# Performance work log

Hardware: AMD Instinct MI355X
Metric: run time of the kernel (lower is better)

Reference implementation:

```python
import jax, jax.numpy as jnp
import numpy as np
import math

B, T, E, H = 64, 256, 1024, 16
HD = E // H  # 64
EPS = 1e-5


def layernorm(x, g, b):
    mu = jnp.mean(x, axis=-1, keepdims=True)
    var = jnp.mean(jnp.square(x - mu), axis=-1, keepdims=True)
    return (x - mu) * jax.lax.rsqrt(var + EPS) * g + b


def setup_inputs() -> dict:
    key = jax.random.key(0)
    ks = jax.random.split(key, 10)
    s = 0.02
    return {
        "x": jax.random.normal(ks[0], (B, T, E), dtype=jnp.float32),
        "ln1_g": jnp.ones((E,), jnp.float32),
        "ln1_b": jnp.zeros((E,), jnp.float32),
        "wk": jax.random.normal(ks[1], (H, E, HD), jnp.float32) * s,
        "wq": jax.random.normal(ks[2], (H, E, HD), jnp.float32) * s,
        "wv": jax.random.normal(ks[3], (H, E, HD), jnp.float32) * s,
        "w_proj": jax.random.normal(ks[4], (E, E), jnp.float32) * s,
        "b_proj": jnp.zeros((E,), jnp.float32),
        "ln2_g": jnp.ones((E,), jnp.float32),
        "ln2_b": jnp.zeros((E,), jnp.float32),
        "w1": jax.random.normal(ks[5], (E, E), jnp.float32) * s,
        "b1": jnp.zeros((E,), jnp.float32),
        "w2": jax.random.normal(ks[6], (E, E), jnp.float32) * s,
        "b2": jnp.zeros((E,), jnp.float32),
    }


def reference(x, ln1_g, ln1_b, wk, wq, wv, w_proj, b_proj, ln2_g, ln2_b, w1, b1, w2, b2):
    # --- multi-head causal attention on LN1(x) ---
    h = layernorm(x, ln1_g, ln1_b)
    k = jnp.einsum('bte,hed->bhtd', h, wk)
    q = jnp.einsum('bte,hed->bhtd', h, wq)
    v = jnp.einsum('bte,hed->bhtd', h, wv)
    # NOTE: original computes k @ q^T (K.Q^T), not the standard Q.K^T -- kept faithful
    scores = jnp.einsum('bhtd,bhsd->bhts', k, q) / math.sqrt(HD)
    mask = jnp.tril(jnp.ones((T, T), dtype=bool))
    scores = jnp.where(mask, scores, -jnp.inf)
    attn_w = jax.nn.softmax(scores, axis=-1)  # dropout = identity in eval
    attn = jnp.einsum('bhts,bhsd->bhtd', attn_w, v)
    attn = attn.transpose(0, 2, 1, 3).reshape(B, T, E)  # concat heads
    x = x + attn @ w_proj + b_proj
    # --- feed-forward on LN2(x) ---
    h2 = layernorm(x, ln2_g, ln2_b)
    ff = jax.nn.relu(h2 @ w1 + b1) @ w2 + b2
    return x + ff
```

## Files before the change

### kernel.cpp

```cpp
#include <hip/hip_runtime.h>

typedef unsigned int u32;
typedef unsigned short u16;
typedef __attribute__((ext_vector_type(8))) short bf16x8;
typedef __attribute__((ext_vector_type(4))) float f32x4;

#define GLOBAL_AS __attribute__((address_space(1)))
#define LDS_AS    __attribute__((address_space(3)))

#define B_   64
#define T_   256
#define E_   1024
#define H_   16
#define HD_  64
#define NTOK (B_*T_)
#define K_   1024
#define LNEPS 1e-5f

__device__ __forceinline__ u16 f2bf(float f){
  u32 x = __float_as_uint(f);
  u32 r = x + 0x7fffu + ((x >> 16) & 1u);
  return (u16)(r >> 16);
}
__device__ __forceinline__ u16 f2bf_trunc(float f){
  return (u16)(__float_as_uint(f) >> 16);
}
__device__ __forceinline__ u32 pack2(float a, float b){
  return (u32)f2bf(a) | ((u32)f2bf(b) << 16);
}

__device__ __forceinline__ void gload16(const u16* g, u16* l){
  __builtin_amdgcn_global_load_lds((const GLOBAL_AS void*)g, (LDS_AS void*)l, 16, 0, 0);
}

__global__ __launch_bounds__(256) void ln_bf16_kernel(
    const float* __restrict__ x, const float* __restrict__ g,
    const float* __restrict__ b, u16* __restrict__ o)
{
  int lane  = threadIdx.x & 63;
  int token = (blockIdx.x << 2) + (threadIdx.x >> 6);
  const float4* xr = (const float4*)(x + (size_t)token * E_);
  float4 v[4];
  float s = 0.f, ss = 0.f;
  #pragma unroll
  for (int i = 0; i < 4; ++i){
    v[i] = xr[lane + 64 * i];
    s += v[i].x + v[i].y + v[i].z + v[i].w;
    ss = fmaf(v[i].x, v[i].x, fmaf(v[i].y, v[i].y,
         fmaf(v[i].z, v[i].z, fmaf(v[i].w, v[i].w, ss))));
  }
  #pragma unroll
  for (int off = 32; off > 0; off >>= 1){
    s  += __shfl_xor(s,  off);
    ss += __shfl_xor(ss, off);
  }
  float mu   = s * (1.f / E_);
  float var  = ss * (1.f / E_) - mu * mu;
  float rstd = rsqrtf(var + LNEPS);
  const float4* gr = (const float4*)g;
  const float4* br = (const float4*)b;
  uint2* orow = (uint2*)(o + (size_t)token * E_);
  #pragma unroll
  for (int i = 0; i < 4; ++i){
    float4 gg = gr[lane + 64 * i], bb = br[lane + 64 * i];
    float y0 = (v[i].x - mu) * rstd * gg.x + bb.x;
    float y1 = (v[i].y - mu) * rstd * gg.y + bb.y;
    float y2 = (v[i].z - mu) * rstd * gg.z + bb.z;
    float y3 = (v[i].w - mu) * rstd * gg.w + bb.w;
    orow[lane + 64 * i] = make_uint2(pack2(y0, y1), pack2(y2, y3));
  }
}

__global__ __launch_bounds__(256) void convq_kernel(
    const float* __restrict__ wk, const float* __restrict__ wq,
    const float* __restrict__ wv, u16* __restrict__ o)
{
  __shared__ float tile[64 * 68];
  const int zh = blockIdx.x, z = zh >> 4, h = zh & 15;
  const int k0 = blockIdx.y << 6;
  const float* w = (z == 0 ? wk : z == 1 ? wq : wv) + (size_t)h * (E_ * HD_);
  const int t = threadIdx.x;
  {
    int kr = t >> 2, d0 = (t & 3) << 4;
    const float4* src = (const float4*)(w + (size_t)(k0 + kr) * HD_ + d0);
    #pragma unroll
    for (int i = 0; i < 4; ++i)
      *(float4*)(tile + kr * 68 + d0 + 4 * i) = src[i];
  }
  __syncthreads();
  {
    const size_t nb32 = (size_t)zh * 32 + (k0 >> 5);
    #pragma unroll
    for (int u = 0; u < 2; ++u) {
      int cid = t * 2 + u;
      int dd = cid >> 3, kc = cid & 7;
      u32 wd[4];
      #pragma unroll
      for (int e2 = 0; e2 < 4; ++e2)
        wd[e2] = pack2(tile[(kc * 8 + 2 * e2) * 68 + dd],
                       tile[(kc * 8 + 2 * e2 + 1) * 68 + dd]);
      u16* dst = o + (nb32 + (kc >> 2)) * 2048 + (size_t)(dd >> 4) * 512
                   + (size_t)(((kc & 3) << 4) + (dd & 15)) * 8;
      *(uint4*)dst = make_uint4(wd[0], wd[1], wd[2], wd[3]);
    }
  }
}

__global__ __launch_bounds__(256) void convt_kernel(
    const float* __restrict__ w, u16* __restrict__ o)
{
  __shared__ float tile[64 * 68];
  const int n0 = blockIdx.x << 6, k0 = blockIdx.y << 6;
  const int t = threadIdx.x;
  {
    int kr = t >> 2, nn = (t & 3) << 4;
    const float4* src = (const float4*)(w + (size_t)(k0 + kr) * E_ + n0 + nn);
    #pragma unroll
    for (int i = 0; i < 4; ++i)
      *(float4*)(tile + kr * 68 + nn + 4 * i) = src[i];
  }
  __syncthreads();
  {
    const size_t nb32 = (size_t)(n0 >> 6) * 32 + (k0 >> 5);
    #pragma unroll
    for (int u = 0; u < 2; ++u) {
      int cid = t * 2 + u;
      int dd = cid >> 3, kc = cid & 7;
      u32 wd[4];
      #pragma unroll
      for (int e2 = 0; e2 < 4; ++e2)
        wd[e2] = pack2(tile[(kc * 8 + 2 * e2) * 68 + dd],
                       tile[(kc * 8 + 2 * e2 + 1) * 68 + dd]);
      u16* dst = o + (nb32 + (kc >> 2)) * 2048 + (size_t)(dd >> 4) * 512
                   + (size_t)(((kc & 3) << 4) + (dd & 15)) * 8;
      *(uint4*)dst = make_uint4(wd[0], wd[1], wd[2], wd[3]);
    }
  }
}

#define MF4(I, AV, BV)                                                               \
  acc[I][0] = __builtin_amdgcn_mfma_f32_16x16x32_bf16(AV, BV[0], acc[I][0], 0, 0, 0);\
  acc[I][1] = __builtin_amdgcn_mfma_f32_16x16x32_bf16(AV, BV[1], acc[I][1], 0, 0, 0);\
  acc[I][2] = __builtin_amdgcn_mfma_f32_16x16x32_bf16(AV, BV[2], acc[I][2], 0, 0, 0);\
  acc[I][3] = __builtin_amdgcn_mfma_f32_16x16x32_bf16(AV, BV[3], acc[I][3], 0, 0, 0);

#define BLOADS(BV, SS) {                                                      \
    const u16* bp_ = Bp + (size_t)(SS) * 2048;                                \
    BV[0] = *(const bf16x8*)(bp_);                                            \
    BV[1] = *(const bf16x8*)(bp_ + 512);                                      \
    BV[2] = *(const bf16x8*)(bp_ + 1024);                                     \
    BV[3] = *(const bf16x8*)(bp_ + 1536);                                     \
  }

#define MSLICE(SLOT, DST, KA, DO_STAGE, BV, BL, VM) {                         \
    const u16* As_ = lds + (SLOT) * 8192;                                     \
    bf16x8 a0 = *(const bf16x8*)(As_ + aoffb);                                \
    bf16x8 a1 = *(const bf16x8*)(As_ + aoffb + 512);                          \
    bf16x8 a2 = *(const bf16x8*)(As_ + aoffb + 1024);                         \
    bf16x8 a3 = *(const bf16x8*)(As_ + aoffb + 1536);                         \
    if (DO_STAGE) {                                                           \
      u16* d_ = lds + (DST) * 8192;                                           \
      gload16(Ag0 + (KA), d_ + tid * 8);                                      \
      gload16(Ag1 + (KA), d_ + 4096 + tid * 8);                               \
    }                                                                         \
    __builtin_amdgcn_s_barrier();                                             \
    asm volatile("s_waitcnt lgkmcnt(0)" ::: "memory");                        \
    __builtin_amdgcn_sched_barrier(0);                                        \
    __builtin_amdgcn_s_setprio(1);                                            \
    MF4(0, a0, BV) MF4(1, a1, BV) MF4(2, a2, BV) MF4(3, a3, BV)               \
    __builtin_amdgcn_s_setprio(0);                                            \
    a0 = *(const bf16x8*)(As_ + aoffb + 2048);                                \
    a1 = *(const bf16x8*)(As_ + aoffb + 2560);                                \
    a2 = *(const bf16x8*)(As_ + aoffb + 3072);                                \
    a3 = *(const bf16x8*)(As_ + aoffb + 3584);                                \
    asm volatile("s_waitcnt lgkmcnt(0)" ::: "memory");                        \
    __builtin_amdgcn_sched_barrier(0);                                        \
    __builtin_amdgcn_s_setprio(1);                                            \
    MF4(4, a0, BV) MF4(5, a1, BV) MF4(6, a2, BV) MF4(7, a3, BV)               \
    __builtin_amdgcn_s_setprio(0);                                            \
    BL;                                                                       \
    VM;                                                                       \
    __builtin_amdgcn_s_barrier();                                             \
    asm volatile("" ::: "memory");                                            \
  }

#define VM12 asm volatile("s_waitcnt vmcnt(12)" ::: "memory")
#define VM10 asm volatile("s_waitcnt vmcnt(10)" ::: "memory")
#define VM8  asm volatile("s_waitcnt vmcnt(8)"  ::: "memory")

template<int MODE>
__global__ __launch_bounds__(512, 2) void mgemm_kernel(
    const u16* __restrict__ A, const u16* __restrict__ Bt,
    const float* __restrict__ bias, const float* __restrict__ resid,
    float* __restrict__ Cf, u16* __restrict__ Cb, u16* __restrict__ Cb2)
{
  __shared__ __align__(16) u16 lds[65536];

  const int tid = threadIdx.x, lane = tid & 63, wid = tid >> 6;
  const int wm = wid >> 2, wn = wid & 3;
  const int l15 = lane & 15, quad = lane >> 4;

  const int b = (int)blockIdx.x;
  const int xcd = b & 7, ib = b >> 3;
  const int row0 = ((xcd << 3) + (ib & 7)) << 8;
  const int col0 = (ib >> 3) << 8;

  const int sc   = (tid & 7) ^ ((tid >> 3) & 7);
  const int srow = 2 * (tid >> 3) + (sc >> 2);
  const int skof = (sc & 3) << 3;
  const u16* Ag0 = A + (size_t)(row0 + srow) * K_ + skof;
  const u16* Ag1 = Ag0 + (size_t)128 * K_;

  const int rhalf = l15 >> 1;
  const int cph   = ((((l15 & 1) << 2) | quad) ^ rhalf);
  const int aoffb = wm * 4096 + rhalf * 64 + cph * 8;

  const u16* Bp = Bt + (size_t)((col0 >> 6) + wn) * 65536 + lane * 8;

  f32x4 acc[8][4];
  #pragma unroll
  for (int i = 0; i < 8; ++i)
    #pragma unroll
    for (int j = 0; j < 4; ++j)
      acc[i][j] = (f32x4){0.f, 0.f, 0.f, 0.f};

  bf16x8 bE[4], bO[4];

  #pragma unroll
  for (int t3 = 0; t3 < 3; ++t3) {
    u16* d_ = lds + t3 * 8192;
    gload16(Ag0 + t3 * 32, d_ + tid * 8);
    gload16(Ag1 + t3 * 32, d_ + 4096 + tid * 8);
  }
  BLOADS(bE, 0)
  BLOADS(bO, 1)
  asm volatile("s_waitcnt vmcnt(12)" ::: "memory");
  __builtin_amdgcn_s_barrier();
  asm volatile("" ::: "memory");

  #pragma unroll 1
  for (int s = 0; s < 28; s += 2) {
    MSLICE(s & 3, (s + 3) & 3, (s + 3) * 32, 1, bE, BLOADS(bE, s + 2), VM12)
    MSLICE((s + 1) & 3, (s + 4) & 3, (s + 4) * 32, 1, bO, BLOADS(bO, s + 3), VM12)
  }
  MSLICE(0, 3, 31 * 32, 1, bE, BLOADS(bE, 30), VM12)
  MSLICE(1, 0, 0,       0, bO, BLOADS(bO, 31), VM10)
  MSLICE(2, 0, 0,       0, bE, (void)0,        VM8 )
  MSLICE(3, 0, 0,       0, bO, (void)0,        (void)0)

  if (MODE == 1 || MODE == 3) {
    const int rbase = row0 + wm * 128;
    #pragma unroll
    for (int j = 0; j < 4; ++j) {
      const int n = col0 + wn * 64 + j * 16 + l15;
      const float bn = bias[n];
      #pragma unroll
      for (int i = 0; i < 8; ++i)
        #pragma unroll
        for (int r = 0; r < 4; ++r) {
          const int row = rbase + i * 16 + quad * 4 + r;
          const size_t idx = (size_t)row * E_ + n;
          float v = acc[i][j][r] + bn;
          if (MODE == 1) Cf[idx] = v + resid[idx];
          else           Cf[idx] = v + Cf[idx];
        }
    }
    return;
  }

  u16* ep = lds + wid * 8192;
  const int nb0 = col0 + wn * 64;

  if (MODE == 2) {
    #pragma unroll
    for (int j = 0; j < 4; ++j) {
      const float bn = bias[nb0 + j * 16 + l15];
      #pragma unroll
      for (int i = 0; i < 8; ++i)
        #pragma unroll
        for (int r = 0; r < 4; ++r)
          ep[(i*16 + quad*4 + r) * 64 + j*16 + l15] =
              f2bf(fmaxf(acc[i][j][r] + bn, 0.f));
    }
    __syncthreads();
    const int rbase = row0 + wm * 128;
    #pragma unroll
    for (int it = 0; it < 16; ++it) {
      const int tl = it * 8 + (lane >> 3), c = lane & 7;
      uint4 v = *(const uint4*)(ep + tl * 64 + c * 8);
      *(uint4*)(Cb + (size_t)(rbase + tl) * E_ + nb0 + c * 8) = v;
    }
    return;
  }

  const int z = nb0 >> 10, hh = (nb0 >> 6) & 15;
  const int rows0 = row0 + wm * 128;
  const int bb = rows0 >> 8, tb0 = rows0 & 255;
  if (z < 2) {
    #pragma unroll
    for (int i = 0; i < 8; ++i)
      #pragma unroll
      for (int j = 0; j < 4; ++j)
        #pragma unroll
        for (int r = 0; r < 4; ++r)
          ep[(i*16 + quad*4 + r) * 64 + j*16 + l15] = f2bf(acc[i][j][r]);
    __syncthreads();
    u16* out = (z == 0 ? Cb : Cb2) + ((size_t)(bb * H_ + hh) * T_ + tb0) * HD_;
    #pragma unroll
    for (int it = 0; it < 16; ++it) {
      const int tl = it * 8 + (lane >> 3), c = lane & 7;
      uint4 v = *(const uint4*)(ep + tl * 64 + c * 8);
      *(uint4*)(out + (size_t)tl * HD_ + c * 8) = v;
    }
  } else {
    #pragma unroll
    for (int i = 0; i < 8; ++i)
      #pragma unroll
      for (int j = 0; j < 4; ++j)
        #pragma unroll
        for (int r = 0; r < 4; ++r) {
          const int tl = i*16 + quad*4 + r, d = j*16 + l15;
          const int phys = (tl >> 3) ^ (d & 15);
          ep[d * 128 + phys * 8 + (tl & 7)] = f2bf(acc[i][j][r]);
        }
    __syncthreads();
    u16* out = (u16*)Cf + ((size_t)(bb * H_ + hh) * HD_) * T_;
    #pragma unroll
    for (int it = 0; it < 16; ++it) {
      const int d = it * 4 + (lane >> 4), c = lane & 15;
      const int phys = c ^ (d & 15);
      uint4 v = *(const uint4*)(ep + d * 128 + phys * 8);
      *(uint4*)(out + (size_t)d * T_ + tb0 + c * 8) = v;
    }
  }
}

__global__ __launch_bounds__(256) void fattn_kernel(
    const u16* __restrict__ kk_, const u16* __restrict__ qq_,
    const u16* __restrict__ vt_, u16* __restrict__ out)
{
  __shared__ __align__(16) u16 Pb[4][64 * 72];
  const int tid = threadIdx.x, lane = tid & 63, wv = tid >> 6;
  const int bh = blockIdx.x * 4 + wv;
  const int tblk = blockIdx.y;
  const int l15 = lane & 15, quad = lane >> 4;
  const u16* kb  = kk_ + (size_t)bh * (T_ * HD_);
  const u16* qb  = qq_ + (size_t)bh * (T_ * HD_);
  const u16* vtb = vt_ + (size_t)bh * (HD_ * T_);
  u16* Pw = Pb[wv];

  bf16x8 kf[4][2];
  #pragma unroll
  for (int i = 0; i < 4; ++i)
    #pragma unroll
    for (int c = 0; c < 2; ++c)
      kf[i][c] = *(const bf16x8*)(kb + (size_t)(tblk*64 + i*16 + l15) * HD_ + c*32 + quad*8);

  f32x4 o[4][4];
  float mrow[4][4], lrow[4][4];
  #pragma unroll
  for (int i = 0; i < 4; ++i) {
    #pragma unroll
    for (int j = 0; j < 4; ++j) o[i][j] = (f32x4){0.f, 0.f, 0.f, 0.f};
    #pragma unroll
    for (int r = 0; r < 4; ++r) { mrow[i][r] = -1e30f; lrow[i][r] = 0.f; }
  }

  for (int sb = 0; sb <= tblk; ++sb) {
    f32x4 S[4][4];
    #pragma unroll
    for (int j = 0; j < 4; ++j) {
      bf16x8 qf0 = *(const bf16x8*)(qb + (size_t)(sb*64 + j*16 + l15) * HD_ +      quad*8);
      bf16x8 qf1 = *(const bf16x8*)(qb + (size_t)(sb*64 + j*16 + l15) * HD_ + 32 + quad*8);
      #pragma unroll
      for (int i = 0; i < 4; ++i) {
        f32x4 t0 = __builtin_amdgcn_mfma_f32_16x16x32_bf16(kf[i][0], qf0,
                       (f32x4){0.f,0.f,0.f,0.f}, 0, 0, 0);
        S[i][j] = __builtin_amdgcn_mfma_f32_16x16x32_bf16(kf[i][1], qf1, t0, 0, 0, 0);
      }
    }
    #pragma unroll
    for (int i = 0; i < 4; ++i)
      #pragma unroll
      for (int j = 0; j < 4; ++j)
        #pragma unroll
        for (int r = 0; r < 4; ++r) {
          float val = S[i][j][r] * 0.125f;
          if (sb == tblk) {
            int tl = i*16 + quad*4 + r, sl = j*16 + l15;
            if (sl > tl) val = -1e30f;
          }
          S[i][j][r] = val;
        }
    #pragma unroll
    for (int i = 0; i < 4; ++i)
      #pragma unroll
      for (int r = 0; r < 4; ++r) {
        float mx = fmaxf(fmaxf(S[i][0][r], S[i][1][r]), fmaxf(S[i][2][r], S[i][3][r]));
        #pragma unroll
        for (int msk = 1; msk < 16; msk <<= 1) mx = fmaxf(mx, __shfl_xor(mx, msk));
        float mn = fmaxf(mrow[i][r], mx);
        float al = __expf(mrow[i][r] - mn);
        mrow[i][r] = mn;
        float sm = 0.f;
        #pragma unroll
        for (int j = 0; j < 4; ++j) {
          float p = __expf(S[i][j][r] - mn);
          S[i][j][r] = p;
          sm += p;
        }
        #pragma unroll
        for (int msk = 1; msk < 16; msk <<= 1) sm += __shfl_xor(sm, msk);
        lrow[i][r] = lrow[i][r] * al + sm;
        #pragma unroll
        for (int jd = 0; jd < 4; ++jd) o[i][jd][r] *= al;
      }
    #pragma unroll
    for (int i = 0; i < 4; ++i)
      #pragma unroll
      for (int j = 0; j < 4; ++j)
        #pragma unroll
        for (int r = 0; r < 4; ++r)
          Pw[(i*16 + quad*4 + r) * 72 + j*16 + l15] = f2bf_trunc(S[i][j][r]);
    __syncthreads();
    bf16x8 pf[4][2];
    #pragma unroll
    for (int i = 0; i < 4; ++i)
      #pragma unroll
      for (int c = 0; c < 2; ++c)
        pf[i][c] = *(const bf16x8*)(Pw + (i*16 + l15) * 72 + c*32 + quad*8);
    #pragma unroll
    for (int jd = 0; jd < 4; ++jd) {
      bf16x8 vf0 = *(const bf16x8*)(vtb + (size_t)(jd*16 + l15) * T_ + sb*64 +      quad*8);
      bf16x8 vf1 = *(const bf16x8*)(vtb + (size_t)(jd*16 + l15) * T_ + sb*64 + 32 + quad*8);
      #pragma unroll
      for (int i = 0; i < 4; ++i) {
        f32x4 t0 = __builtin_amdgcn_mfma_f32_16x16x32_bf16(pf[i][0], vf0, o[i][jd], 0, 0, 0);
        o[i][jd] = __builtin_amdgcn_mfma_f32_16x16x32_bf16(pf[i][1], vf1, t0, 0, 0, 0);
      }
    }
    __syncthreads();
  }

  #pragma unroll
  for (int i = 0; i < 4; ++i)
    #pragma unroll
    for (int r = 0; r < 4; ++r) {
      float inv = 1.0f / lrow[i][r];
      #pragma unroll
      for (int jd = 0; jd < 4; ++jd)
        Pw[(i*16 + quad*4 + r) * 72 + jd*16 + l15] = f2bf(o[i][jd][r] * inv);
    }
  __syncthreads();
  {
    const int b = bh >> 4, h = bh & 15;
    const uint4* pr = (const uint4*)(Pw + lane * 72);
    uint4* og = (uint4*)(out + ((size_t)(b * T_ + tblk*64 + lane)) * E_ + h * HD_);
    #pragma unroll
    for (int k = 0; k < 8; ++k) og[k] = pr[k];
  }
}

extern "C" void kernel_launch(void* const* d_in, const int* in_sizes, int n_in,
                              void* d_out, int out_size, void* d_ws, size_t ws_size,
                              hipStream_t stream) {
  const float* x     = (const float*)d_in[0];
  const float* ln1g  = (const float*)d_in[1];
  const float* ln1b  = (const float*)d_in[2];
  const float* wk    = (const float*)d_in[3];
  const float* wq    = (const float*)d_in[4];
  const float* wv    = (const float*)d_in[5];
  const float* wproj = (const float*)d_in[6];
  const float* bproj = (const float*)d_in[7];
  const float* ln2g  = (const float*)d_in[8];
  const float* ln2b  = (const float*)d_in[9];
  const float* w1    = (const float*)d_in[10];
  const float* b1    = (const float*)d_in[11];
  const float* w2    = (const float*)d_in[12];
  const float* b2    = (const float*)d_in[13];
  float* outp = (float*)d_out;

  char* ws = (char*)d_ws;
  const size_t MB = 1024 * 1024;
  u16* wqkvT  = (u16*)(ws);
  u16* wprojT = (u16*)(ws + 6 * MB);
  u16* w1T    = (u16*)(ws + 8 * MB);
  u16* w2T    = (u16*)(ws + 10 * MB);
  u16* hb     = (u16*)(ws + 16 * MB);
  u16* kbuf   = (u16*)(ws + 48 * MB);
  u16* qbuf   = (u16*)(ws + 80 * MB);
  u16* vtbuf  = (u16*)d_out;

  convq_kernel<<<dim3(48, 16), 256, 0, stream>>>(wk, wq, wv, wqkvT);
  convt_kernel<<<dim3(16, 16), 256, 0, stream>>>(wproj, wprojT);
  convt_kernel<<<dim3(16, 16), 256, 0, stream>>>(w1, w1T);
  convt_kernel<<<dim3(16, 16), 256, 0, stream>>>(w2, w2T);

  ln_bf16_kernel<<<NTOK/4, 256, 0, stream>>>(x, ln1g, ln1b, hb);
  mgemm_kernel<0><<<768, 512, 0, stream>>>(
      hb, wqkvT, nullptr, nullptr, (float*)vtbuf, kbuf, qbuf);
  fattn_kernel<<<dim3(B_*H_/4, 4), 256, 0, stream>>>(kbuf, qbuf, vtbuf, hb);
  mgemm_kernel<1><<<256, 512, 0, stream>>>(
      hb, wprojT, bproj, x, outp, nullptr, nullptr);
  ln_bf16_kernel<<<NTOK/4, 256, 0, stream>>>(outp, ln2g, ln2b, kbuf);
  mgemm_kernel<2><<<256, 512, 0, stream>>>(
      kbuf, w1T, b1, nullptr, nullptr, qbuf, nullptr);
  mgemm_kernel<3><<<256, 512, 0, stream>>>(
      qbuf, w2T, b2, nullptr, outp, nullptr, nullptr);
}
```

Measured before the change: 527.0 us.

## Prefetch next-slice A fragments across barrier in GEMM, drop attention syncthreads

Reworks the GEMM main loop so A fragments for the next k-slice are read from LDS during the current slice's MFMAs, with register double-buffering. This removes the barrier and lgkmcnt wait that sat before each slice's first MFMAs, and the vmcnt thresholds are retuned to match. The attention kernel also drops several __syncthreads around its per-wave P staging buffer, assuming each wave only touches its own Pw region. The cost is extra registers and a risk of LDS read/write races if the slot timing or the per-wave ownership assumptions are wrong.

```diff
diff --git a/kernel.cpp b/kernel.cpp
--- a/kernel.cpp
+++ b/kernel.cpp
@@ -152,41 +152,42 @@
     BV[3] = *(const bf16x8*)(bp_ + 1536);                                     \
   }
 
-#define MSLICE(SLOT, DST, KA, DO_STAGE, BV, BL, VM) {                         \
+#define MSLICE2(SLOT, NSLOT, KA, DO_STAGE, DO_NXT, DO_BL, BS, ACUR, ATMP, ANXT, BV, BNV, VM) { \
     const u16* As_ = lds + (SLOT) * 8192;                                     \
-    bf16x8 a0 = *(const bf16x8*)(As_ + aoffb);                                \
-    bf16x8 a1 = *(const bf16x8*)(As_ + aoffb + 512);                          \
-    bf16x8 a2 = *(const bf16x8*)(As_ + aoffb + 1024);                         \
-    bf16x8 a3 = *(const bf16x8*)(As_ + aoffb + 1536);                         \
+          \
+    ATMP[0] = *(const bf16x8*)(As_ + aoffb + 2048);                           \
+    ATMP[1] = *(const bf16x8*)(As_ + aoffb + 2560);                           \
+    ATMP[2] = *(const bf16x8*)(As_ + aoffb + 3072);                           \
+    ATMP[3] = *(const bf16x8*)(As_ + aoffb + 3584);                           \
     if (DO_STAGE) {                                                           \
-      u16* d_ = lds + (DST) * 8192;                                           \
+      u16* d_ = lds + (((SLOT) + 3) & 3) * 8192;                              \
       gload16(Ag0 + (KA), d_ + tid * 8);                                      \
       gload16(Ag1 + (KA), d_ + 4096 + tid * 8);                               \
     }                                                                         \
-    __builtin_amdgcn_s_barrier();                                             \
-    asm volatile("s_waitcnt lgkmcnt(0)" ::: "memory");                        \
-    __builtin_amdgcn_sched_barrier(0);                                        \
     __builtin_amdgcn_s_setprio(1);                                            \
-    MF4(0, a0, BV) MF4(1, a1, BV) MF4(2, a2, BV) MF4(3, a3, BV)               \
+    MF4(0, ACUR[0], BV) MF4(1, ACUR[1], BV) MF4(2, ACUR[2], BV) MF4(3, ACUR[3], BV) \
     __builtin_amdgcn_s_setprio(0);                                            \
-    a0 = *(const bf16x8*)(As_ + aoffb + 2048);                                \
-    a1 = *(const bf16x8*)(As_ + aoffb + 2560);                                \
-    a2 = *(const bf16x8*)(As_ + aoffb + 3072);                                \
-    a3 = *(const bf16x8*)(As_ + aoffb + 3584);                                \
-    asm volatile("s_waitcnt lgkmcnt(0)" ::: "memory");                        \
-    __builtin_amdgcn_sched_barrier(0);                                        \
+             \
+    if (DO_NXT) {                                                             \
+      const u16* An_ = lds + (NSLOT) * 8192;                                  \
+      ANXT[0] = *(const bf16x8*)(An_ + aoffb);                                \
+      ANXT[1] = *(const bf16x8*)(An_ + aoffb + 512);                          \
+      ANXT[2] = *(const bf16x8*)(An_ + aoffb + 1024);                         \
+      ANXT[3] = *(const bf16x8*)(An_ + aoffb + 1536);                         \
+    }                                                                         \
     __builtin_amdgcn_s_setprio(1);                                            \
-    MF4(4, a0, BV) MF4(5, a1, BV) MF4(6, a2, BV) MF4(7, a3, BV)               \
+    MF4(4, ATMP[0], BV) MF4(5, ATMP[1], BV) MF4(6, ATMP[2], BV) MF4(7, ATMP[3], BV) \
     __builtin_amdgcn_s_setprio(0);                                            \
-    BL;                                                                       \
+    if (DO_BL) { BLOADS(BNV, BS) }                                            \
     VM;                                                                       \
     __builtin_amdgcn_s_barrier();                                             \
+    __builtin_amdgcn_sched_barrier(0);                                        \
     asm volatile("" ::: "memory");                                            \
   }
 
-#define VM12 asm volatile("s_waitcnt vmcnt(12)" ::: "memory")
 #define VM10 asm volatile("s_waitcnt vmcnt(10)" ::: "memory")
 #define VM8  asm volatile("s_waitcnt vmcnt(8)"  ::: "memory")
+#define VM4  asm volatile("s_waitcnt vmcnt(4)"  ::: "memory")
 
 template<int MODE>
 __global__ __launch_bounds__(512, 2) void mgemm_kernel(
@@ -224,7 +225,7 @@
     for (int j = 0; j < 4; ++j)
       acc[i][j] = (f32x4){0.f, 0.f, 0.f, 0.f};
 
-  bf16x8 bE[4], bO[4];
+  bf16x8 aA[4], aB[4], aT[4], bE[4], bO[4];
 
   #pragma unroll
   for (int t3 = 0; t3 < 3; ++t3) {
@@ -234,19 +235,25 @@
   }
   BLOADS(bE, 0)
   BLOADS(bO, 1)
-  asm volatile("s_waitcnt vmcnt(12)" ::: "memory");
+  asm volatile("s_waitcnt vmcnt(10)" ::: "memory");
   __builtin_amdgcn_s_barrier();
+  __builtin_amdgcn_sched_barrier(0);
   asm volatile("" ::: "memory");
+
+  aA[0] = *(const bf16x8*)(lds + aoffb);
+  aA[1] = *(const bf16x8*)(lds + aoffb + 512);
+  aA[2] = *(const bf16x8*)(lds + aoffb + 1024);
+  aA[3] = *(const bf16x8*)(lds + aoffb + 1536);
 
   #pragma unroll 1
   for (int s = 0; s < 28; s += 2) {
-    MSLICE(s & 3, (s + 3) & 3, (s + 3) * 32, 1, bE, BLOADS(bE, s + 2), VM12)
-    MSLICE((s + 1) & 3, (s + 4) & 3, (s + 4) * 32, 1, bO, BLOADS(bO, s + 3), VM12)
-  }
-  MSLICE(0, 3, 31 * 32, 1, bE, BLOADS(bE, 30), VM12)
-  MSLICE(1, 0, 0,       0, bO, BLOADS(bO, 31), VM10)
-  MSLICE(2, 0, 0,       0, bE, (void)0,        VM8 )
-  MSLICE(3, 0, 0,       0, bO, (void)0,        (void)0)
+    MSLICE2(s & 3, (s + 1) & 3, (s + 3) * 32, 1, 1, 1, s + 2, aA, aT, aB, bE, bE, VM10)
+    MSLICE2((s + 1) & 3, (s + 2) & 3, (s + 4) * 32, 1, 1, 1, s + 3, aB, aT, aA, bO, bO, VM10)
+  }
+  MSLICE2(0, 1, 31 * 32, 1, 1, 1, 30, aA, aT, aB, bE, bE, VM10)
+  MSLICE2(1, 2, 0,       0, 1, 1, 31, aB, aT, aA, bO, bO, VM8 )
+  MSLICE2(2, 3, 0,       0, 1, 0, 0,  aA, aT, aB, bE, bE, VM4 )
+  MSLICE2(3, 0, 0,       0, 0, 0, 0,  aB, aT, aA, bO, bO, (void)0)
 
   if (MODE == 1 || MODE == 3) {
     const int rbase = row0 + wm * 128;
@@ -422,7 +429,6 @@
         #pragma unroll
         for (int r = 0; r < 4; ++r)
           Pw[(i*16 + quad*4 + r) * 72 + j*16 + l15] = f2bf_trunc(S[i][j][r]);
-    __syncthreads();
     bf16x8 pf[4][2];
     #pragma unroll
     for (int i = 0; i < 4; ++i)
@@ -439,7 +445,6 @@
         o[i][jd] = __builtin_amdgcn_mfma_f32_16x16x32_bf16(pf[i][1], vf1, t0, 0, 0, 0);
       }
     }
-    __syncthreads();
   }
 
   #pragma unroll
@@ -451,7 +456,6 @@
       for (int jd = 0; jd < 4; ++jd)
         Pw[(i*16 + quad*4 + r) * 72 + jd*16 + l15] = f2bf(o[i][jd][r] * inv);
     }
-  __syncthreads();
   {
     const int b = bh >> 4, h = bh & 15;
     const uint4* pr = (const uint4*)(Pw + lane * 72);
```

Result: faster. 513.1 us (-2.7%).
